# Optimization experiments

Hardware: AMD Instinct MI355X
Metric: run time of the kernel (lower is better)

The kernel has to match this reference:

```python
import jax, jax.numpy as jnp
import numpy as np

B, T, D = 4, 2048, 256   # batch, temporal_scale, input_dim
H = 8                    # num_heads (hard-coded in module)
DH = D // H              # head dim
DFF = 512                # dim_feedforward (hard-coded)
WIN = 9                  # window_size
EPS = 1e-5               # LayerNorm eps


def _window_mask(t, h, w):
    # True = masked (disallowed). Each row j allows columns clip(j - w//2 + k, 0, t-1), k in [0, w).
    rows = jnp.arange(t)[:, None]                                   # [t,1]
    cols = jnp.clip(rows - w // 2 + jnp.arange(w)[None, :], 0, t - 1)  # [t,w]
    allowed = jnp.zeros((t, t), dtype=bool).at[rows, cols].set(True)
    # local_len == num_heads == 8: every head gets the same window mask
    return jnp.broadcast_to(~allowed, (h, t, t))                    # [H,T,T]


def setup_inputs() -> dict:
    key = jax.random.key(0)
    ks = jax.random.split(key, 6)
    s = 0.05
    return {
        "features": jax.random.normal(ks[0], (B, T, D), jnp.float32),
        "w_qkv": jax.random.normal(ks[1], (3 * D, D), jnp.float32) * s,
        "b_qkv": jnp.zeros((3 * D,), jnp.float32),
        "w_out": jax.random.normal(ks[2], (D, D), jnp.float32) * s,
        "b_out": jnp.zeros((D,), jnp.float32),
        "w1": jax.random.normal(ks[3], (DFF, D), jnp.float32) * s,
        "b1": jnp.zeros((DFF,), jnp.float32),
        "w2": jax.random.normal(ks[4], (D, DFF), jnp.float32) * s,
        "b2": jnp.zeros((D,), jnp.float32),
        "g1": jnp.ones((D,), jnp.float32),
        "be1": jnp.zeros((D,), jnp.float32),
        "g2": jnp.ones((D,), jnp.float32),
        "be2": jnp.zeros((D,), jnp.float32),
        "mask": _window_mask(T, H, WIN),
    }


def _layernorm(x, g, b):
    mu = jnp.mean(x, axis=-1, keepdims=True)
    var = jnp.var(x, axis=-1, keepdims=True)
    return (x - mu) * jax.lax.rsqrt(var + EPS) * g + b


def reference(features, w_qkv, b_qkv, w_out, b_out, w1, b1, w2, b2,
              g1, be1, g2, be2, mask):
    b, t, d = features.shape
    # --- windowed multi-head self-attention (dropout = eval-mode identity) ---
    qkv = features @ w_qkv.T + b_qkv                         # [b,t,3d]
    q, k, v = jnp.split(qkv, 3, axis=-1)
    split_heads = lambda x: x.reshape(b, t, H, DH).transpose(0, 2, 1, 3)  # [b,H,t,dh]
    q, k, v = split_heads(q), split_heads(k), split_heads(v)
    scores = jnp.einsum('bhqd,bhkd->bhqk', q, k) / jnp.sqrt(jnp.float32(DH))
    scores = jnp.where(mask[None], -jnp.inf, scores)         # mask True = disallowed
    attn = jax.nn.softmax(scores, axis=-1)                   # [b,H,t,t]
    o = jnp.einsum('bhqk,bhkd->bhqd', attn, v)
    o = o.transpose(0, 2, 1, 3).reshape(b, t, d)
    o = o @ w_out.T + b_out
    # --- residual + norm1 ---
    x = _layernorm(features + o, g1, be1)
    # --- FFN (relu) + residual + norm2 ---
    ff = jax.nn.relu(x @ w1.T + b1) @ w2.T + b2
    return _layernorm(x + ff, g2, be2)
```

## Files before the change

kernel.cpp:

```cpp
#include <hip/hip_runtime.h>
#include <math.h>

#define T_LEN 2048
#define LN_EPS 1e-5f
#define M_ROWS 8192

using u16x8  = __attribute__((ext_vector_type(8))) unsigned short;
using bf16x8 = __attribute__((ext_vector_type(8))) short;
using f32x4  = __attribute__((ext_vector_type(4))) float;

__device__ __forceinline__ unsigned short f2bf(float f) {
    unsigned int u = __float_as_uint(f);
    u += 0x7FFFu + ((u >> 16) & 1u);
    return (unsigned short)(u >> 16);
}
__device__ __forceinline__ float bf2f(unsigned short u) {
    return __uint_as_float(((unsigned int)u) << 16);
}
__device__ __forceinline__ u16x8 pack8(float4 a, float4 c) {
    u16x8 p;
    p[0] = f2bf(a.x); p[1] = f2bf(a.y); p[2] = f2bf(a.z); p[3] = f2bf(a.w);
    p[4] = f2bf(c.x); p[5] = f2bf(c.y); p[6] = f2bf(c.z); p[7] = f2bf(c.w);
    return p;
}
__device__ __forceinline__ void gload16(const void* g, void* l) {
    __builtin_amdgcn_global_load_lds(
        (const __attribute__((address_space(1))) unsigned int*)g,
        (__attribute__((address_space(3))) unsigned int*)l, 16, 0, 0);
}
__device__ __forceinline__ void bar_vm4() {
    asm volatile("s_waitcnt vmcnt(4)" ::: "memory");
    __builtin_amdgcn_s_barrier();
}
__device__ __forceinline__ void bar_vm0() {
    asm volatile("s_waitcnt vmcnt(0)" ::: "memory");
    __builtin_amdgcn_s_barrier();
}

__global__ __launch_bounds__(512) void kv_gemm_f32(
    const float* __restrict__ A, const float* __restrict__ Wqkv,
    const float* __restrict__ bias,
    const float* __restrict__ wo, const float* __restrict__ w1,
    const float* __restrict__ w2,
    unsigned short* __restrict__ KV, unsigned short* __restrict__ wconv)
{
    __shared__ char sm[2][32768];

    const int tid = threadIdx.x, lane = tid & 63, wid = tid >> 6;
    const int wr = wid >> 2, wcl = wid & 3;
    const int m0 = blockIdx.x * 128, n0 = blockIdx.y * 128;

    {
        const int bid = blockIdx.y * 64 + blockIdx.x;
        const int g = bid * 512 + tid;
        if (g < 49152) {
            const int e = g * 8;
            const float* src; int off;
            if (e < 65536)       { src = Wqkv; off = 0; }
            else if (e < 131072) { src = wo;   off = 65536; }
            else if (e < 262144) { src = w1;   off = 131072; }
            else                 { src = w2;   off = 262144; }
            const float4 a = *(const float4*)(src + (e - off));
            const float4 c = *(const float4*)(src + (e - off) + 4);
            *(u16x8*)(wconv + e) = pack8(a, c);
        }
    }

    float4 ld[4][2];
    auto LOADR = [&](int k0) {
        #pragma unroll
        for (int j = 0; j < 4; ++j) {
            const int i = j * 512 + tid;
            const float* src;
            if (i < 1024) {
                const int row = i >> 3, k8 = i & 7;
                src = A + (size_t)(m0 + row) * 256 + k0 + k8 * 8;
            } else {
                const int ii = i - 1024;
                const int row = ii >> 3, k8 = ii & 7;
                src = Wqkv + (size_t)(256 + n0 + row) * 256 + k0 + k8 * 8;
            }
            ld[j][0] = *(const float4*)src;
            ld[j][1] = *(const float4*)(src + 4);
        }
    };
    auto CWRITE = [&](char* buf) {
        #pragma unroll
        for (int j = 0; j < 4; ++j) {
            const int i = j * 512 + tid;
            const u16x8 p = pack8(ld[j][0], ld[j][1]);
            if (i < 1024) {
                const int row = i >> 3, k8 = i & 7;
                *(u16x8*)(buf + ((row * 128 + k8 * 16) ^ ((row & 7) << 4))) = p;
            } else {
                const int ii = i - 1024;
                const int row = ii >> 3, k8 = ii & 7;
                *(u16x8*)(buf + 16384 + ((row * 128 + k8 * 16) ^ ((row & 7) << 4))) = p;
            }
        }
    };

    f32x4 acc[4][2];
    #pragma unroll
    for (int m = 0; m < 4; ++m)
        #pragma unroll
        for (int n = 0; n < 2; ++n) acc[m][n] = (f32x4)(0.f);

    LOADR(0);
    CWRITE(sm[0]);
    __syncthreads();

    #pragma unroll
    for (int k = 0; k < 4; ++k) {
        if (k < 3) LOADR((k + 1) * 64);
        char* As = sm[k & 1];
        char* Ws = sm[k & 1] + 16384;
        #pragma unroll
        for (int ks = 0; ks < 2; ++ks) {
            bf16x8 af[4], bfr[2];
            #pragma unroll
            for (int m = 0; m < 4; ++m) {
                const int row = wr * 64 + m * 16 + (lane & 15);
                const int off = (row * 128 + ks * 64 + (lane >> 4) * 16) ^ ((row & 7) << 4);
                af[m] = *(const bf16x8*)(As + off);
            }
            #pragma unroll
            for (int n = 0; n < 2; ++n) {
                const int row = wcl * 32 + n * 16 + (lane & 15);
                const int off = (row * 128 + ks * 64 + (lane >> 4) * 16) ^ ((row & 7) << 4);
                bfr[n] = *(const bf16x8*)(Ws + off);
            }
            #pragma unroll
            for (int m = 0; m < 4; ++m)
                #pragma unroll
                for (int n = 0; n < 2; ++n)
                    acc[m][n] = __builtin_amdgcn_mfma_f32_16x16x32_bf16(
                        af[m], bfr[n], acc[m][n], 0, 0, 0);
        }
        if (k < 3) CWRITE(sm[(k + 1) & 1]);
        __syncthreads();
    }

    #pragma unroll
    for (int n = 0; n < 2; ++n) {
        const int c = n0 + wcl * 32 + n * 16 + (lane & 15);
        const float bv = bias[256 + c];
        #pragma unroll
        for (int m = 0; m < 4; ++m) {
            const int rbase = m0 + wr * 64 + m * 16 + ((lane >> 4) << 2);
            #pragma unroll
            for (int j = 0; j < 4; ++j)
                KV[(size_t)(rbase + j) * 512 + c] = f2bf(acc[m][n][j] + bv);
        }
    }
}

__global__ __launch_bounds__(512) void tail_fused_pipe2(
    const unsigned short* __restrict__ kv, const unsigned short* __restrict__ wconv,
    const float* __restrict__ features, const float* __restrict__ b_qkv,
    const float* __restrict__ b_out,
    const float* __restrict__ g1, const float* __restrict__ be1,
    const float* __restrict__ b1, const float* __restrict__ b2,
    const float* __restrict__ g2, const float* __restrict__ be2,
    float* __restrict__ out)
{
    __shared__ __align__(16) char sm[149504];
    char* smA = sm;
    char* smH = sm + 114688;
    char* smF = smH;
    char* smQ = smH + 16384;
    float* part = (float*)(sm + 147456);

    const int tid = threadIdx.x, lane = tid & 63, wid = tid >> 6;
    const int m0 = blockIdx.x * 32;
    const int b = m0 >> 11, t0 = m0 & 2047;

    const unsigned short* Wq = wconv;
    const unsigned short* Wo = wconv + 65536;
    const unsigned short* W1 = wconv + 131072;
    const unsigned short* W2 = wconv + 262144;

    auto stbuf = [&](int i) -> char* { return sm + 16384 + (i % 3) * 32768; };
    auto NSTAGE = [&](int i) {
        if (i >= 24) return;
        const unsigned short* W; int ldk, ro, k0;
        if (i < 4)       { W = Wq; ldk = 256; ro = 0;                    k0 = i * 64; }
        else if (i < 8)  { W = Wo; ldk = 256; ro = 0;                    k0 = (i - 4) * 64; }
        else if (i < 16) { W = W1; ldk = 256; ro = ((i - 8) >> 2) * 256; k0 = ((i - 8) & 3) * 64; }
        else             { W = W2; ldk = 512; ro = 0;                    k0 = (i - 16) * 64; }
        char* dst = stbuf(i);
        #pragma unroll
        for (int j = 0; j < 4; ++j) {
            const int ii = j * 512 + tid, row = ii >> 3, k8 = (ii & 7) ^ (row & 7);
            gload16(W + (size_t)(ro + row) * ldk + k0 + k8 * 8, dst + ii * 16);
        }
    };

    NSTAGE(0); NSTAGE(1);

    #pragma unroll
    for (int j = 0; j < 2; ++j) {
        const int i = j * 512 + tid;
        const int e = i >> 5, ch = i & 31;
        const float* src = features + ((size_t)(b * T_LEN + t0 + e)) * 256 + ch * 8;
        const float4 a = *(const float4*)src;
        const float4 c = *(const float4*)(src + 4);
        *(u16x8*)(smF + e * 512 + ((ch ^ (e & 7)) << 4)) = pack8(a, c);
    }
    __syncthreads();

    {
        f32x4 acc[2][2];
        #pragma unroll
        for (int m = 0; m < 2; ++m)
            #pragma unroll
            for (int n = 0; n < 2; ++n) acc[m][n] = (f32x4)(0.f);

        #pragma unroll
        for (int i = 0; i < 4; ++i) {
            NSTAGE(i + 2);
            char* Bs = stbuf(i);
            #pragma unroll
            for (int ks = 0; ks < 2; ++ks) {
                bf16x8 af[2], bfr[2];
                #pragma unroll
                for (int m = 0; m < 2; ++m) {
                    const int r = m * 16 + (lane & 15);
                    const int ch = i * 8 + ks * 4 + (lane >> 4);
                    af[m] = *(const bf16x8*)(smF + r * 512 + ((ch ^ (r & 7)) << 4));
                }
                #pragma unroll
                for (int n = 0; n < 2; ++n) {
                    const int rB = wid * 32 + n * 16 + (lane & 15);
                    bfr[n] = *(const bf16x8*)(Bs + rB * 128
                             + (((ks * 4 + (lane >> 4)) ^ (rB & 7)) << 4));
                }
                #pragma unroll
                for (int m = 0; m < 2; ++m)
                    #pragma unroll
                    for (int n = 0; n < 2; ++n)
                        acc[m][n] = __builtin_amdgcn_mfma_f32_16x16x32_bf16(
                            af[m], bfr[n], acc[m][n], 0, 0, 0);
            }
            bar_vm4();
        }
        #pragma unroll
        for (int n = 0; n < 2; ++n) {
            const int c = wid * 32 + n * 16 + (lane & 15);
            const float bv = b_qkv[c];
            #pragma unroll
            for (int m = 0; m < 2; ++m) {
                const int rb = m * 16 + ((lane >> 4) << 2);
                #pragma unroll
                for (int j = 0; j < 4; ++j) {
                    const int r = rb + j;
                    const int addr = r * 512 + (((c >> 3) ^ (r & 7)) << 4) + ((c & 7) << 1);
                    *(unsigned short*)(smQ + addr) = f2bf(acc[m][n][j] + bv);
                }
            }
        }
    }
    __syncthreads();

    {
        const int half = tid & 1, p = tid >> 1;
        const int h = p & 7, tl = p >> 3;
        const int t = t0 + tl;
        const unsigned short* kvb = kv + (size_t)b * T_LEN * 512;

        float q[16];
        #pragma unroll
        for (int jj = 0; jj < 2; ++jj) {
            const int ch = h * 4 + half * 2 + jj;
            u16x8 u = *(const u16x8*)(smQ + tl * 512 + ((ch ^ (tl & 7)) << 4));
            #pragma unroll
            for (int e = 0; e < 8; ++e) q[jj * 8 + e] = bf2f(u[e]);
        }
        const unsigned short* kbase = kvb + h * 32 + half * 16;
        const unsigned short* vbase = kvb + 256 + h * 32 + half * 16;

        float sc[9], mx = -1e30f;
        #pragma unroll
        for (int j = 0; j < 9; ++j) {
            const int kr0 = t - 4 + j;
            const int krm = min(max(kr0, 0), T_LEN - 1);
            const unsigned short* kr = kbase + (size_t)krm * 512;
            float d = 0.f;
            #pragma unroll
            for (int jj = 0; jj < 2; ++jj) {
                u16x8 u = *(const u16x8*)(kr + jj * 8);
                #pragma unroll
                for (int e = 0; e < 8; ++e) d += q[jj * 8 + e] * bf2f(u[e]);
            }
            d += __shfl_xor(d, 1);
            sc[j] = (kr0 == krm) ? d * 0.17677669529663687f : -1e30f;
            mx = fmaxf(mx, sc[j]);
        }
        float sum = 0.f;
        #pragma unroll
        for (int j = 0; j < 9; ++j) { sc[j] = expf(sc[j] - mx); sum += sc[j]; }
        const float inv = 1.f / sum;

        float ov[16] = {};
        #pragma unroll
        for (int j = 0; j < 9; ++j) {
            const float pj = sc[j] * inv;
            const int krm = min(max(t - 4 + j, 0), T_LEN - 1);
            const unsigned short* vr = vbase + (size_t)krm * 512;
            #pragma unroll
            for (int jj = 0; jj < 2; ++jj) {
                u16x8 u = *(const u16x8*)(vr + jj * 8);
                #pragma unroll
                for (int e = 0; e < 8; ++e) ov[jj * 8 + e] += pj * bf2f(u[e]);
            }
        }
        #pragma unroll
        for (int jj = 0; jj < 2; ++jj) {
            u16x8 p8;
            #pragma unroll
            for (int e = 0; e < 8; ++e) p8[e] = f2bf(ov[jj * 8 + e]);
            const int ch = h * 4 + half * 2 + jj;
            *(u16x8*)(smA + tl * 512 + ((ch ^ (tl & 7)) << 4)) = p8;
        }
    }
    __syncthreads();

    float xres[2][2][4];

    {
        f32x4 acc[2][2];
        #pragma unroll
        for (int m = 0; m < 2; ++m)
            #pragma unroll
            for (int n = 0; n < 2; ++n) acc[m][n] = (f32x4)(0.f);

        #pragma unroll
        for (int i = 4; i < 8; ++i) {
            NSTAGE(i + 2);
            const int kk = i - 4;
            char* Bs = stbuf(i);
            #pragma unroll
            for (int ks = 0; ks < 2; ++ks) {
                bf16x8 af[2], bfr[2];
                #pragma unroll
                for (int m = 0; m < 2; ++m) {
                    const int r = m * 16 + (lane & 15);
                    const int ch = kk * 8 + ks * 4 + (lane >> 4);
                    af[m] = *(const bf16x8*)(smA + r * 512 + ((ch ^ (r & 7)) << 4));
                }
                #pragma unroll
                for (int n = 0; n < 2; ++n) {
                    const int rB = wid * 32 + n * 16 + (lane & 15);
                    bfr[n] = *(const bf16x8*)(Bs + rB * 128
                             + (((ks * 4 + (lane >> 4)) ^ (rB & 7)) << 4));
                }
                #pragma unroll
                for (int m = 0; m < 2; ++m)
                    #pragma unroll
                    for (int n = 0; n < 2; ++n)
                        acc[m][n] = __builtin_amdgcn_mfma_f32_16x16x32_bf16(
                            af[m], bfr[n], acc[m][n], 0, 0, 0);
            }
            bar_vm4();
        }

        float v[2][2][4], s[2][4], sq[2][4];
        #pragma unroll
        for (int m = 0; m < 2; ++m)
            #pragma unroll
            for (int j = 0; j < 4; ++j) { s[m][j] = 0.f; sq[m][j] = 0.f; }
        #pragma unroll
        for (int n = 0; n < 2; ++n) {
            const int c = wid * 32 + n * 16 + (lane & 15);
            const float bv = b_out[c];
            #pragma unroll
            for (int m = 0; m < 2; ++m) {
                const int rb = m * 16 + ((lane >> 4) << 2);
                #pragma unroll
                for (int j = 0; j < 4; ++j) {
                    float x = acc[m][n][j] + bv
                            + features[(size_t)(m0 + rb + j) * 256 + c];
                    v[m][n][j] = x; s[m][j] += x; sq[m][j] += x * x;
                }
            }
        }
        #pragma unroll
        for (int m = 0; m < 2; ++m)
            #pragma unroll
            for (int j = 0; j < 4; ++j) {
                #pragma unroll
                for (int msk = 1; msk <= 8; msk <<= 1) {
                    s[m][j]  += __shfl_xor(s[m][j], msk);
                    sq[m][j] += __shfl_xor(sq[m][j], msk);
                }
                if ((lane & 15) == 0) {
                    const int r = m * 16 + ((lane >> 4) << 2) + j;
                    part[(wid * 32 + r) * 2 + 0] = s[m][j];
                    part[(wid * 32 + r) * 2 + 1] = sq[m][j];
                }
            }
        __syncthreads();
        #pragma unroll
        for (int m = 0; m < 2; ++m) {
            const int rb = m * 16 + ((lane >> 4) << 2);
            #pragma unroll
            for (int j = 0; j < 4; ++j) {
                const int r = rb + j;
                float S = 0.f, SQ = 0.f;
                #pragma unroll
                for (int w = 0; w < 8; ++w) {
                    S += part[(w * 32 + r) * 2 + 0]; SQ += part[(w * 32 + r) * 2 + 1];
                }
                const float mean = S * (1.f / 256.f);
                const float var  = SQ * (1.f / 256.f) - mean * mean;
                const float rstd = rsqrtf(var + LN_EPS);
                #pragma unroll
                for (int n = 0; n < 2; ++n) {
                    const int c = wid * 32 + n * 16 + (lane & 15);
                    const float o = (v[m][n][j] - mean) * rstd * g1[c] + be1[c];
                    xres[m][n][j] = o;
                    const int addr = r * 512 + (((c >> 3) ^ (r & 7)) << 4) + ((c & 7) << 1);
                    *(unsigned short*)(smA + addr) = f2bf(o);
                }
            }
        }
    }
    __syncthreads();

    {
        f32x4 acc[2][2];
        #pragma unroll
        for (int m = 0; m < 2; ++m)
            #pragma unroll
            for (int n = 0; n < 2; ++n) acc[m][n] = (f32x4)(0.f);

        #pragma unroll
        for (int i = 8; i < 16; ++i) {
            NSTAGE(i + 2);
            const int kk = (i - 8) & 3, half = (i - 8) >> 2;
            char* Bs = stbuf(i);
            #pragma unroll
            for (int ks = 0; ks < 2; ++ks) {
                bf16x8 af[2], bfr[2];
                #pragma unroll
                for (int m = 0; m < 2; ++m) {
                    const int r = m * 16 + (lane & 15);
                    const int ch = kk * 8 + ks * 4 + (lane >> 4);
                    af[m] = *(const bf16x8*)(smA + r * 512 + ((ch ^ (r & 7)) << 4));
                }
                #pragma unroll
                for (int n = 0; n < 2; ++n) {
                    const int rB = wid * 32 + n * 16 + (lane & 15);
                    bfr[n] = *(const bf16x8*)(Bs + rB * 128
                             + (((ks * 4 + (lane >> 4)) ^ (rB & 7)) << 4));
                }
                #pragma unroll
                for (int m = 0; m < 2; ++m)
                    #pragma unroll
                    for (int n = 0; n < 2; ++n)
                        acc[m][n] = __builtin_amdgcn_mfma_f32_16x16x32_bf16(
                            af[m], bfr[n], acc[m][n], 0, 0, 0);
            }
            bar_vm4();
            if (kk == 3) {
                #pragma unroll
                for (int n = 0; n < 2; ++n) {
                    const int c = half * 256 + wid * 32 + n * 16 + (lane & 15);
                    const float bv = b1[c];
                    #pragma unroll
                    for (int m = 0; m < 2; ++m) {
                        const int rb = m * 16 + ((lane >> 4) << 2);
                        #pragma unroll
                        for (int j = 0; j < 4; ++j) {
                            const int rr = rb + j;
                            const int addr = rr * 1024 + (((c >> 3) ^ (rr & 7)) << 4)
                                           + ((c & 7) << 1);
                            *(unsigned short*)(smH + addr) =
                                f2bf(fmaxf(acc[m][n][j] + bv, 0.f));
                        }
                    }
                }
                #pragma unroll
                for (int m = 0; m < 2; ++m)
                    #pragma unroll
                    for (int n = 0; n < 2; ++n) acc[m][n] = (f32x4)(0.f);
            }
        }
    }
    __syncthreads();

    {
        f32x4 acc[2][2];
        #pragma unroll
        for (int m = 0; m < 2; ++m)
            #pragma unroll
            for (int n = 0; n < 2; ++n) acc[m][n] = (f32x4)(0.f);

        #pragma unroll
        for (int i = 16; i < 24; ++i) {
            NSTAGE(i + 2);
            const int k = i - 16;
            char* Bs = stbuf(i);
            #pragma unroll
            for (int ks = 0; ks < 2; ++ks) {
                bf16x8 af[2], bfr[2];
                #pragma unroll
                for (int m = 0; m < 2; ++m) {
                    const int r = m * 16 + (lane & 15);
                    const int ch = k * 8 + ks * 4 + (lane >> 4);
                    af[m] = *(const bf16x8*)(smH + r * 1024 + ((ch ^ (r & 7)) << 4));
                }
                #pragma unroll
                for (int n = 0; n < 2; ++n) {
                    const int rB = wid * 32 + n * 16 + (lane & 15);
                    bfr[n] = *(const bf16x8*)(Bs + rB * 128
                             + (((ks * 4 + (lane >> 4)) ^ (rB & 7)) << 4));
                }
                #pragma unroll
                for (int m = 0; m < 2; ++m)
                    #pragma unroll
                    for (int n = 0; n < 2; ++n)
                        acc[m][n] = __builtin_amdgcn_mfma_f32_16x16x32_bf16(
                            af[m], bfr[n], acc[m][n], 0, 0, 0);
            }
            if (i + 2 < 24) bar_vm4(); else bar_vm0();
        }

        float v[2][2][4], s[2][4], sq[2][4];
        #pragma unroll
        for (int m = 0; m < 2; ++m)
            #pragma unroll
            for (int j = 0; j < 4; ++j) { s[m][j] = 0.f; sq[m][j] = 0.f; }
        #pragma unroll
        for (int n = 0; n < 2; ++n) {
            const int c = wid * 32 + n * 16 + (lane & 15);
            const float bv = b2[c];
            #pragma unroll
            for (int m = 0; m < 2; ++m) {
                #pragma unroll
                for (int j = 0; j < 4; ++j) {
                    float x = acc[m][n][j] + bv + xres[m][n][j];
                    v[m][n][j] = x; s[m][j] += x; sq[m][j] += x * x;
                }
            }
        }
        #pragma unroll
        for (int m = 0; m < 2; ++m)
            #pragma unroll
            for (int j = 0; j < 4; ++j) {
                #pragma unroll
                for (int msk = 1; msk <= 8; msk <<= 1) {
                    s[m][j]  += __shfl_xor(s[m][j], msk);
                    sq[m][j] += __shfl_xor(sq[m][j], msk);
                }
                if ((lane & 15) == 0) {
                    const int r = m * 16 + ((lane >> 4) << 2) + j;
                    part[(wid * 32 + r) * 2 + 0] = s[m][j];
                    part[(wid * 32 + r) * 2 + 1] = sq[m][j];
                }
            }
        __syncthreads();
        #pragma unroll
        for (int m = 0; m < 2; ++m) {
            const int rb = m * 16 + ((lane >> 4) << 2);
            #pragma unroll
            for (int j = 0; j < 4; ++j) {
                const int r = rb + j;
                float S = 0.f, SQ = 0.f;
                #pragma unroll
                for (int w = 0; w < 8; ++w) {
                    S += part[(w * 32 + r) * 2 + 0]; SQ += part[(w * 32 + r) * 2 + 1];
                }
                const float mean = S * (1.f / 256.f);
                const float var  = SQ * (1.f / 256.f) - mean * mean;
                const float rstd = rsqrtf(var + LN_EPS);
                #pragma unroll
                for (int n = 0; n < 2; ++n) {
                    const int c = wid * 32 + n * 16 + (lane & 15);
                    out[(size_t)(m0 + r) * 256 + c] =
                        (v[m][n][j] - mean) * rstd * g2[c] + be2[c];
                }
            }
        }
    }
}

extern "C" void kernel_launch(void* const* d_in, const int* in_sizes, int n_in,
                              void* d_out, int out_size, void* d_ws, size_t ws_size,
                              hipStream_t stream) {
    const float* features = (const float*)d_in[0];
    const float* w_qkv    = (const float*)d_in[1];
    const float* b_qkv    = (const float*)d_in[2];
    const float* w_out    = (const float*)d_in[3];
    const float* b_out    = (const float*)d_in[4];
    const float* w1       = (const float*)d_in[5];
    const float* b1       = (const float*)d_in[6];
    const float* w2       = (const float*)d_in[7];
    const float* b2       = (const float*)d_in[8];
    const float* g1       = (const float*)d_in[9];
    const float* be1      = (const float*)d_in[10];
    const float* g2       = (const float*)d_in[11];
    const float* be2      = (const float*)d_in[12];

    unsigned short* wsu = (unsigned short*)d_ws;
    unsigned short* wconv = wsu;
    unsigned short* kvbf  = wsu + 393216;

    kv_gemm_f32<<<dim3(64, 4), 512, 0, stream>>>(
        features, w_qkv, b_qkv, w_out, w1, w2, kvbf, wconv);
    tail_fused_pipe2<<<M_ROWS / 32, 512, 0, stream>>>(
        kvbf, wconv, features, b_qkv, b_out, g1, be1, b1, b2, g2, be2,
        (float*)d_out);
}
```

Before: 37.40 us.

## Load weight B-fragments directly into registers instead of LDS staging pipeline

Drops the triple-buffered global-to-LDS weight staging in the fused tail kernel. Each wave now loads its weight fragments straight from global memory into registers, prefetching the next GEMM's weights while the current stage runs. This removes the vmcnt barriers and shrinks shared memory from about 146KB to 50KB, which could let more blocks fit per CU. The cost is much higher register pressure (16 bf16x8 per buffer, with two buffers live), which risks spills or lower occupancy, and uncoalesced per-lane global loads of the weights.

Result: slower. 49.03 us (+31.1%).

```diff
diff --git a/kernel.cpp b/kernel.cpp
--- a/kernel.cpp
+++ b/kernel.cpp
@@ -23,17 +23,8 @@
     p[4] = f2bf(c.x); p[5] = f2bf(c.y); p[6] = f2bf(c.z); p[7] = f2bf(c.w);
     return p;
 }
-__device__ __forceinline__ void gload16(const void* g, void* l) {
-    __builtin_amdgcn_global_load_lds(
-        (const __attribute__((address_space(1))) unsigned int*)g,
-        (__attribute__((address_space(3))) unsigned int*)l, 16, 0, 0);
-}
-__device__ __forceinline__ void bar_vm4() {
-    asm volatile("s_waitcnt vmcnt(4)" ::: "memory");
-    __builtin_amdgcn_s_barrier();
-}
-__device__ __forceinline__ void bar_vm0() {
-    asm volatile("s_waitcnt vmcnt(0)" ::: "memory");
+__device__ __forceinline__ void bar_lds() {
+    asm volatile("s_waitcnt lgkmcnt(0)" ::: "memory");
     __builtin_amdgcn_s_barrier();
 }
 
@@ -155,7 +146,7 @@
     }
 }
 
-__global__ __launch_bounds__(512) void tail_fused_pipe2(
+__global__ __launch_bounds__(512) void tail_fused_regB(
     const unsigned short* __restrict__ kv, const unsigned short* __restrict__ wconv,
     const float* __restrict__ features, const float* __restrict__ b_qkv,
     const float* __restrict__ b_out,
@@ -164,39 +155,31 @@
     const float* __restrict__ g2, const float* __restrict__ be2,
     float* __restrict__ out)
 {
-    __shared__ __align__(16) char sm[149504];
+    __shared__ __align__(16) char sm[51200];
     char* smA = sm;
-    char* smH = sm + 114688;
+    char* smH = sm + 16384;
     char* smF = smH;
     char* smQ = smH + 16384;
-    float* part = (float*)(sm + 147456);
+    float* part = (float*)(sm + 49152);
 
     const int tid = threadIdx.x, lane = tid & 63, wid = tid >> 6;
     const int m0 = blockIdx.x * 32;
     const int b = m0 >> 11, t0 = m0 & 2047;
+    const int rowB = wid * 32 + (lane & 15);
+    const int kofs = (lane >> 4) * 8;
 
     const unsigned short* Wq = wconv;
     const unsigned short* Wo = wconv + 65536;
     const unsigned short* W1 = wconv + 131072;
     const unsigned short* W2 = wconv + 262144;
 
-    auto stbuf = [&](int i) -> char* { return sm + 16384 + (i % 3) * 32768; };
-    auto NSTAGE = [&](int i) {
-        if (i >= 24) return;
-        const unsigned short* W; int ldk, ro, k0;
-        if (i < 4)       { W = Wq; ldk = 256; ro = 0;                    k0 = i * 64; }
-        else if (i < 8)  { W = Wo; ldk = 256; ro = 0;                    k0 = (i - 4) * 64; }
-        else if (i < 16) { W = W1; ldk = 256; ro = ((i - 8) >> 2) * 256; k0 = ((i - 8) & 3) * 64; }
-        else             { W = W2; ldk = 512; ro = 0;                    k0 = (i - 16) * 64; }
-        char* dst = stbuf(i);
-        #pragma unroll
-        for (int j = 0; j < 4; ++j) {
-            const int ii = j * 512 + tid, row = ii >> 3, k8 = (ii & 7) ^ (row & 7);
-            gload16(W + (size_t)(ro + row) * ldk + k0 + k8 * 8, dst + ii * 16);
-        }
-    };
-
-    NSTAGE(0); NSTAGE(1);
+    bf16x8 Bq[8][2];
+    #pragma unroll
+    for (int kc = 0; kc < 8; ++kc)
+        #pragma unroll
+        for (int n = 0; n < 2; ++n)
+            Bq[kc][n] = *(const bf16x8*)(Wq + (size_t)(rowB + n * 16) * 256
+                                         + kc * 32 + kofs);
 
     #pragma unroll
     for (int j = 0; j < 2; ++j) {
@@ -207,7 +190,9 @@
         const float4 c = *(const float4*)(src + 4);
         *(u16x8*)(smF + e * 512 + ((ch ^ (e & 7)) << 4)) = pack8(a, c);
     }
-    __syncthreads();
+    bar_lds();
+
+    bf16x8 Bo[8][2];
 
     {
         f32x4 acc[2][2];
@@ -217,33 +202,29 @@
             for (int n = 0; n < 2; ++n) acc[m][n] = (f32x4)(0.f);
 
         #pragma unroll
-        for (int i = 0; i < 4; ++i) {
-            NSTAGE(i + 2);
-            char* Bs = stbuf(i);
-            #pragma unroll
-            for (int ks = 0; ks < 2; ++ks) {
-                bf16x8 af[2], bfr[2];
-                #pragma unroll
-                for (int m = 0; m < 2; ++m) {
-                    const int r = m * 16 + (lane & 15);
-                    const int ch = i * 8 + ks * 4 + (lane >> 4);
-                    af[m] = *(const bf16x8*)(smF + r * 512 + ((ch ^ (r & 7)) << 4));
-                }
-                #pragma unroll
-                for (int n = 0; n < 2; ++n) {
-                    const int rB = wid * 32 + n * 16 + (lane & 15);
-                    bfr[n] = *(const bf16x8*)(Bs + rB * 128
-                             + (((ks * 4 + (lane >> 4)) ^ (rB & 7)) << 4));
-                }
-                #pragma unroll
-                for (int m = 0; m < 2; ++m)
-                    #pragma unroll
-                    for (int n = 0; n < 2; ++n)
-                        acc[m][n] = __builtin_amdgcn_mfma_f32_16x16x32_bf16(
-                            af[m], bfr[n], acc[m][n], 0, 0, 0);
-            }
-            bar_vm4();
-        }
+        for (int kc = 0; kc < 8; ++kc) {
+            bf16x8 af[2];
+            #pragma unroll
+            for (int m = 0; m < 2; ++m) {
+                const int r = m * 16 + (lane & 15);
+                const int ch = kc * 4 + (lane >> 4);
+                af[m] = *(const bf16x8*)(smF + r * 512 + ((ch ^ (r & 7)) << 4));
+            }
+            #pragma unroll
+            for (int m = 0; m < 2; ++m)
+                #pragma unroll
+                for (int n = 0; n < 2; ++n)
+                    acc[m][n] = __builtin_amdgcn_mfma_f32_16x16x32_bf16(
+                        af[m], Bq[kc][n], acc[m][n], 0, 0, 0);
+        }
+
+        #pragma unroll
+        for (int kc = 0; kc < 8; ++kc)
+            #pragma unroll
+            for (int n = 0; n < 2; ++n)
+                Bo[kc][n] = *(const bf16x8*)(Wo + (size_t)(rowB + n * 16) * 256
+                                             + kc * 32 + kofs);
+
         #pragma unroll
         for (int n = 0; n < 2; ++n) {
             const int c = wid * 32 + n * 16 + (lane & 15);
@@ -260,7 +241,7 @@
             }
         }
     }
-    __syncthreads();
+    bar_lds();
 
     {
         const int half = tid & 1, p = tid >> 1;
@@ -323,9 +304,10 @@
             *(u16x8*)(smA + tl * 512 + ((ch ^ (tl & 7)) << 4)) = p8;
         }
     }
-    __syncthreads();
+    bar_lds();
 
     float xres[2][2][4];
+    bf16x8 B1a[8][2];
 
     {
         f32x4 acc[2][2];
@@ -335,34 +317,28 @@
             for (int n = 0; n < 2; ++n) acc[m][n] = (f32x4)(0.f);
 
         #pragma unroll
-        for (int i = 4; i < 8; ++i) {
-            NSTAGE(i + 2);
-            const int kk = i - 4;
-            char* Bs = stbuf(i);
-            #pragma unroll
-            for (int ks = 0; ks < 2; ++ks) {
-                bf16x8 af[2], bfr[2];
-                #pragma unroll
-                for (int m = 0; m < 2; ++m) {
-                    const int r = m * 16 + (lane & 15);
-                    const int ch = kk * 8 + ks * 4 + (lane >> 4);
-                    af[m] = *(const bf16x8*)(smA + r * 512 + ((ch ^ (r & 7)) << 4));
-                }
-                #pragma unroll
-                for (int n = 0; n < 2; ++n) {
-                    const int rB = wid * 32 + n * 16 + (lane & 15);
-                    bfr[n] = *(const bf16x8*)(Bs + rB * 128
-                             + (((ks * 4 + (lane >> 4)) ^ (rB & 7)) << 4));
-                }
-                #pragma unroll
-                for (int m = 0; m < 2; ++m)
-                    #pragma unroll
-                    for (int n = 0; n < 2; ++n)
-                        acc[m][n] = __builtin_amdgcn_mfma_f32_16x16x32_bf16(
-                            af[m], bfr[n], acc[m][n], 0, 0, 0);
-            }
-            bar_vm4();
-        }
+        for (int kc = 0; kc < 8; ++kc) {
+            bf16x8 af[2];
+            #pragma unroll
+            for (int m = 0; m < 2; ++m) {
+                const int r = m * 16 + (lane & 15);
+                const int ch = kc * 4 + (lane >> 4);
+                af[m] = *(const bf16x8*)(smA + r * 512 + ((ch ^ (r & 7)) << 4));
+            }
+            #pragma unroll
+            for (int m = 0; m < 2; ++m)
+                #pragma unroll
+                for (int n = 0; n < 2; ++n)
+                    acc[m][n] = __builtin_amdgcn_mfma_f32_16x16x32_bf16(
+                        af[m], Bo[kc][n], acc[m][n], 0, 0, 0);
+        }
+
+        #pragma unroll
+        for (int kc = 0; kc < 8; ++kc)
+            #pragma unroll
+            for (int n = 0; n < 2; ++n)
+                B1a[kc][n] = *(const bf16x8*)(W1 + (size_t)(rowB + n * 16) * 256
+                                              + kc * 32 + kofs);
 
         float v[2][2][4], s[2][4], sq[2][4];
         #pragma unroll
@@ -399,7 +375,7 @@
                     part[(wid * 32 + r) * 2 + 1] = sq[m][j];
                 }
             }
-        __syncthreads();
+        bar_lds();
         #pragma unroll
         for (int m = 0; m < 2; ++m) {
             const int rb = m * 16 + ((lane >> 4) << 2);
@@ -425,105 +401,118 @@
             }
         }
     }
-    __syncthreads();
+    bar_lds();
 
     {
-        f32x4 acc[2][2];
-        #pragma unroll
-        for (int m = 0; m < 2; ++m)
-            #pragma unroll
-            for (int n = 0; n < 2; ++n) acc[m][n] = (f32x4)(0.f);
-
-        #pragma unroll
-        for (int i = 8; i < 16; ++i) {
-            NSTAGE(i + 2);
-            const int kk = (i - 8) & 3, half = (i - 8) >> 2;
-            char* Bs = stbuf(i);
-            #pragma unroll
-            for (int ks = 0; ks < 2; ++ks) {
-                bf16x8 af[2], bfr[2];
+        bf16x8 B1b[8][2];
+        #pragma unroll
+        for (int kc = 0; kc < 8; ++kc)
+            #pragma unroll
+            for (int n = 0; n < 2; ++n)
+                B1b[kc][n] = *(const bf16x8*)(W1 + (size_t)(256 + rowB + n * 16) * 256
+                                              + kc * 32 + kofs);
+
+        bf16x8 B2a[8][2];
+
+        #pragma unroll
+        for (int nh = 0; nh < 2; ++nh) {
+            f32x4 acc[2][2];
+            #pragma unroll
+            for (int m = 0; m < 2; ++m)
+                #pragma unroll
+                for (int n = 0; n < 2; ++n) acc[m][n] = (f32x4)(0.f);
+
+            #pragma unroll
+            for (int kc = 0; kc < 8; ++kc) {
+                bf16x8 af[2];
                 #pragma unroll
                 for (int m = 0; m < 2; ++m) {
                     const int r = m * 16 + (lane & 15);
-                    const int ch = kk * 8 + ks * 4 + (lane >> 4);
+                    const int ch = kc * 4 + (lane >> 4);
                     af[m] = *(const bf16x8*)(smA + r * 512 + ((ch ^ (r & 7)) << 4));
-                }
-                #pragma unroll
-                for (int n = 0; n < 2; ++n) {
-                    const int rB = wid * 32 + n * 16 + (lane & 15);
-                    bfr[n] = *(const bf16x8*)(Bs + rB * 128
-                             + (((ks * 4 + (lane >> 4)) ^ (rB & 7)) << 4));
                 }
                 #pragma unroll
                 for (int m = 0; m < 2; ++m)
                     #pragma unroll
                     for (int n = 0; n < 2; ++n)
                         acc[m][n] = __builtin_amdgcn_mfma_f32_16x16x32_bf16(
-                            af[m], bfr[n], acc[m][n], 0, 0, 0);
-            }
-            bar_vm4();
-            if (kk == 3) {
-                #pragma unroll
-                for (int n = 0; n < 2; ++n) {
-                    const int c = half * 256 + wid * 32 + n * 16 + (lane & 15);
-                    const float bv = b1[c];
-                    #pragma unroll
-                    for (int m = 0; m < 2; ++m) {
-                        const int rb = m * 16 + ((lane >> 4) << 2);
-                        #pragma unroll
-                        for (int j = 0; j < 4; ++j) {
-                            const int rr = rb + j;
-                            const int addr = rr * 1024 + (((c >> 3) ^ (rr & 7)) << 4)
-                                           + ((c & 7) << 1);
-                            *(unsigned short*)(smH + addr) =
-                                f2bf(fmaxf(acc[m][n][j] + bv, 0.f));
-                        }
-                    }
-                }
-                #pragma unroll
-                for (int m = 0; m < 2; ++m)
-                    #pragma unroll
-                    for (int n = 0; n < 2; ++n) acc[m][n] = (f32x4)(0.f);
-            }
-        }
-    }
-    __syncthreads();
-
-    {
-        f32x4 acc[2][2];
-        #pragma unroll
-        for (int m = 0; m < 2; ++m)
-            #pragma unroll
-            for (int n = 0; n < 2; ++n) acc[m][n] = (f32x4)(0.f);
-
-        #pragma unroll
-        for (int i = 16; i < 24; ++i) {
-            NSTAGE(i + 2);
-            const int k = i - 16;
-            char* Bs = stbuf(i);
-            #pragma unroll
-            for (int ks = 0; ks < 2; ++ks) {
-                bf16x8 af[2], bfr[2];
-                #pragma unroll
-                for (int m = 0; m < 2; ++m) {
-                    const int r = m * 16 + (lane & 15);
-                    const int ch = k * 8 + ks * 4 + (lane >> 4);
-                    af[m] = *(const bf16x8*)(smH + r * 1024 + ((ch ^ (r & 7)) << 4));
-                }
-                #pragma unroll
-                for (int n = 0; n < 2; ++n) {
-                    const int rB = wid * 32 + n * 16 + (lane & 15);
-                    bfr[n] = *(const bf16x8*)(Bs + rB * 128
-                             + (((ks * 4 + (lane >> 4)) ^ (rB & 7)) << 4));
-                }
-                #pragma unroll
-                for (int m = 0; m < 2; ++m)
+                            af[m], nh == 0 ? B1a[kc][n] : B1b[kc][n],
+                            acc[m][n], 0, 0, 0);
+            }
+            if (nh == 0) {
+                #pragma unroll
+                for (int kc = 0; kc < 8; ++kc)
                     #pragma unroll
                     for (int n = 0; n < 2; ++n)
-                        acc[m][n] = __builtin_amdgcn_mfma_f32_16x16x32_bf16(
-                            af[m], bfr[n], acc[m][n], 0, 0, 0);
-            }
-            if (i + 2 < 24) bar_vm4(); else bar_vm0();
+                        B2a[kc][n] = *(const bf16x8*)(W2 + (size_t)(rowB + n * 16) * 512
+                                                      + kc * 32 + kofs);
+            }
+            #pragma unroll
+            for (int n = 0; n < 2; ++n) {
+                const int c = nh * 256 + wid * 32 + n * 16 + (lane & 15);
+                const float bv = b1[c];
+                #pragma unroll
+                for (int m = 0; m < 2; ++m) {
+                    const int rb = m * 16 + ((lane >> 4) << 2);
+                    #pragma unroll
+                    for (int j = 0; j < 4; ++j) {
+                        const int rr = rb + j;
+                        const int addr = rr * 1024 + (((c >> 3) ^ (rr & 7)) << 4)
+                                       + ((c & 7) << 1);
+                        *(unsigned short*)(smH + addr) =
+                            f2bf(fmaxf(acc[m][n][j] + bv, 0.f));
+                    }
+                }
+            }
+        }
+
+        bar_lds();
+
+        f32x4 acc[2][2];
+        #pragma unroll
+        for (int m = 0; m < 2; ++m)
+            #pragma unroll
+            for (int n = 0; n < 2; ++n) acc[m][n] = (f32x4)(0.f);
+
+        bf16x8 B2b[8][2];
+        #pragma unroll
+        for (int kc = 0; kc < 8; ++kc)
+            #pragma unroll
+            for (int n = 0; n < 2; ++n)
+                B2b[kc][n] = *(const bf16x8*)(W2 + (size_t)(rowB + n * 16) * 512
+                                              + 256 + kc * 32 + kofs);
+
+        #pragma unroll
+        for (int kc = 0; kc < 8; ++kc) {
+            bf16x8 af[2];
+            #pragma unroll
+            for (int m = 0; m < 2; ++m) {
+                const int r = m * 16 + (lane & 15);
+                const int ch = kc * 4 + (lane >> 4);
+                af[m] = *(const bf16x8*)(smH + r * 1024 + ((ch ^ (r & 7)) << 4));
+            }
+            #pragma unroll
+            for (int m = 0; m < 2; ++m)
+                #pragma unroll
+                for (int n = 0; n < 2; ++n)
+                    acc[m][n] = __builtin_amdgcn_mfma_f32_16x16x32_bf16(
+                        af[m], B2a[kc][n], acc[m][n], 0, 0, 0);
+        }
+        #pragma unroll
+        for (int kc = 0; kc < 8; ++kc) {
+            bf16x8 af[2];
+            #pragma unroll
+            for (int m = 0; m < 2; ++m) {
+                const int r = m * 16 + (lane & 15);
+                const int ch = (kc + 8) * 4 + (lane >> 4);
+                af[m] = *(const bf16x8*)(smH + r * 1024 + ((ch ^ (r & 7)) << 4));
+            }
+            #pragma unroll
+            for (int m = 0; m < 2; ++m)
+                #pragma unroll
+                for (int n = 0; n < 2; ++n)
+                    acc[m][n] = __builtin_amdgcn_mfma_f32_16x16x32_bf16(
+                        af[m], B2b[kc][n], acc[m][n], 0, 0, 0);
         }
 
         float v[2][2][4], s[2][4], sq[2][4];
@@ -559,7 +548,7 @@
                     part[(wid * 32 + r) * 2 + 1] = sq[m][j];
                 }
             }
-        __syncthreads();
+        bar_lds();
         #pragma unroll
         for (int m = 0; m < 2; ++m) {
             const int rb = m * 16 + ((lane >> 4) << 2);
@@ -608,7 +597,7 @@
 
     kv_gemm_f32<<<dim3(64, 4), 512, 0, stream>>>(
         features, w_qkv, b_qkv, w_out, w1, w2, kvbf, wconv);
-    tail_fused_pipe2<<<M_ROWS / 32, 512, 0, stream>>>(
+    tail_fused_regB<<<M_ROWS / 32, 512, 0, stream>>>(
         kvbf, wconv, features, b_qkv, b_out, g1, be1, b1, b2, g2, be2,
         (float*)d_out);
 }
```
